# Performance work log

Measured on AMD Instinct MI355X. Metric: run time of the kernel, lower is better.

## Reference

```python
import jax, jax.numpy as jnp
import numpy as np

B, HP, WP, C = 64, 16, 32, 512   # batch, rows, cols, cnn_feature_size
H = 512                          # hidden_size
L = 2                            # num_layers
MAXH = 32


def setup_inputs() -> dict:
    key = jax.random.key(0)
    ks = jax.random.split(key, 11)
    s = 0.05  # keep gates out of saturation
    return {
        "features":   jax.random.normal(ks[0], (B, HP, WP, C), jnp.float32),
        "pos_emb_fw": jax.random.normal(ks[1], (MAXH + 1, L * 2 * H), jnp.float32) * s,
        "pos_emb_bw": jax.random.normal(ks[2], (MAXH + 1, L * 2 * H), jnp.float32) * s,
        "Wi_fw": jax.random.normal(ks[3], (L, C, 4 * H), jnp.float32) * s,
        "Wh_fw": jax.random.normal(ks[4], (L, H, 4 * H), jnp.float32) * s,
        "bi_fw": jax.random.normal(ks[5], (L, 4 * H), jnp.float32) * s,
        "bh_fw": jax.random.normal(ks[6], (L, 4 * H), jnp.float32) * s,
        "Wi_bw": jax.random.normal(ks[7], (L, C, 4 * H), jnp.float32) * s,
        "Wh_bw": jax.random.normal(ks[8], (L, H, 4 * H), jnp.float32) * s,
        "bi_bw": jax.random.normal(ks[9], (L, 4 * H), jnp.float32) * s,
        "bh_bw": jax.random.normal(ks[10], (L, 4 * H), jnp.float32) * s,
    }


def _stacked_lstm_scan(xs, h0, c0, Wi, Wh, b):
    """xs: (T, N, C); h0, c0: (L, N, H); returns (T, N, H) top-layer outputs."""
    def step(carry, x_t):
        hs, cs = carry
        inp = x_t
        new_h, new_c = [], []
        for l in range(Wi.shape[0]):
            gates = inp @ Wi[l] + hs[l] @ Wh[l] + b[l]          # (N, 4H)
            i_g, f_g, o_g, g_g = jnp.split(gates, 4, axis=-1)   # gate order as in torch chunk
            c_n = jax.nn.sigmoid(f_g) * cs[l] + jax.nn.sigmoid(i_g) * jnp.tanh(g_g)
            h_n = jax.nn.sigmoid(o_g) * jnp.tanh(c_n)
            new_h.append(h_n); new_c.append(c_n)
            inp = h_n
        return (jnp.stack(new_h), jnp.stack(new_c)), inp
    _, ys = jax.lax.scan(step, (h0, c0), xs)
    return ys


def _init_state(pos_emb, row_idx, n, l, h):
    # pos_emb[row_idx]: (N, L*2*H) laid out as [h_1, c_1, ..., h_L, c_L]
    e = pos_emb[row_idx].reshape(n, l, 2, h)
    return e[:, :, 0].transpose(1, 0, 2), e[:, :, 1].transpose(1, 0, 2)  # (L, N, H) each


def reference(features, pos_emb_fw, pos_emb_bw,
              Wi_fw, Wh_fw, bi_fw, bh_fw,
              Wi_bw, Wh_bw, bi_bw, bh_bw):
    b, hp, wp, c = features.shape
    l, _, h4 = Wi_fw.shape
    h = h4 // 4
    n = b * hp  # rows are independent -> fuse into one scan batch

    # (B, Hp, Wp, C) -> (Wp, B*Hp, C), time-major
    xs = features.transpose(2, 0, 1, 3).reshape(wp, n, c)
    # row index i+1 per flattened (b, row) element
    row_idx = jnp.tile(jnp.arange(1, hp + 1), b)  # (N,)

    h0f, c0f = _init_state(pos_emb_fw, row_idx, n, l, h)
    out_fw = _stacked_lstm_scan(xs, h0f, c0f, Wi_fw, Wh_fw, bi_fw + bh_fw)

    h0b, c0b = _init_state(pos_emb_bw, row_idx, n, l, h)
    out_bw = jnp.flip(
        _stacked_lstm_scan(jnp.flip(xs, 0), h0b, c0b, Wi_bw, Wh_bw, bi_bw + bh_bw), 0)

    ctx = jnp.concatenate([out_fw, out_bw], axis=-1)        # (Wp, N, 2H)
    ctx = ctx.reshape(wp, b, hp, 2 * h).transpose(1, 2, 0, 3)  # (B, Hp, Wp, 2H)
    return ctx.reshape(b, hp * wp, 2 * h)
```

## Files before the change

kernel.cpp:

```cpp
#include <hip/hip_runtime.h>
#include <hip/hip_bf16.h>
#include <stdint.h>

#define B_    64
#define HP_   16
#define WP_   32
#define CH_   512
#define HS_   512
#define NSEQ  1024
#define G4    2048
#define KTOT  1024

typedef __hip_bfloat16 bf16_t;
typedef __bf16 bf16x8 __attribute__((ext_vector_type(8)));
typedef float  f32x4  __attribute__((ext_vector_type(4)));

#define WT_OFF   0
#define XBF_OFF  16777216
#define HBUF_OFF 50331648
#define CBUF_OFF 58720256
#define PB_OFF   67108864
#define HB_ELEMS (2*2*1024*512)

__device__ __forceinline__ float sigf(float x) {
    return 1.0f / (1.0f + __expf(-x));
}
__device__ __forceinline__ float tanhfast(float x) {
    x = fminf(fmaxf(x, -15.0f), 15.0f);
    float e = __expf(-2.0f * x);
    return (1.0f - e) / (1.0f + e);
}

__device__ __forceinline__ void gload16(const bf16_t* g, bf16_t* l) {
    __builtin_amdgcn_global_load_lds(
        (const __attribute__((address_space(1))) void*)g,
        (__attribute__((address_space(3))) void*)l, 16, 0, 0);
}

__global__ void k_prep_w(const float* __restrict__ Wi_fw, const float* __restrict__ Wh_fw,
                         const float* __restrict__ Wi_bw, const float* __restrict__ Wh_bw,
                         bf16_t* __restrict__ Wt) {
    int bxi = blockIdx.x;
    int cb = bxi & 63;
    int kb = (bxi >> 6) & 31;
    int u  = bxi >> 11;
    int l  = u >> 1, dir = u & 1;
    const float* Wi = dir ? Wi_bw : Wi_fw;
    const float* Wh = dir ? Wh_bw : Wh_fw;
    int k0 = kb * 32;
    const float* src = (k0 < 512) ? (Wi + (size_t)l*512*2048 + (size_t)k0*2048)
                                  : (Wh + (size_t)l*512*2048 + (size_t)(k0-512)*2048);
    int jblk = cb >> 2, g = cb & 3;
    int sc0 = g*512 + jblk*32;
    int cp0 = cb * 32;
    __shared__ float ld[32][33];
    int tx = threadIdx.x & 31, ty = threadIdx.x >> 5;
#pragma unroll
    for (int i = 0; i < 4; ++i) {
        int kr = ty + i*8;
        ld[kr][tx] = src[(size_t)kr*2048 + sc0 + tx];
    }
    __syncthreads();
#pragma unroll
    for (int i = 0; i < 4; ++i) {
        int cl = ty + i*8;
        Wt[((size_t)u*G4 + cp0 + cl)*KTOT + k0 + tx] = __float2bfloat16(ld[tx][cl]);
    }
}

__global__ void k_prep_bias(const float* __restrict__ bi_fw, const float* __restrict__ bh_fw,
                            const float* __restrict__ bi_bw, const float* __restrict__ bh_bw,
                            float* __restrict__ pb) {
    int id = blockIdx.x * 256 + threadIdx.x;
    if (id >= 4*G4) return;
    int u = id >> 11, cp = id & 2047;
    int l = u >> 1, dir = u & 1;
    int jblk = cp >> 7, rr = cp & 127, g = rr >> 5, jin = rr & 31;
    int col = g*512 + jblk*32 + jin;
    const float* bi = dir ? bi_bw : bi_fw;
    const float* bh = dir ? bh_bw : bh_fw;
    pb[id] = bi[l*G4 + col] + bh[l*G4 + col];
}

__global__ void k_convert_x(const float* __restrict__ f, bf16_t* __restrict__ xbf) {
    int id = blockIdx.x * 256 + threadIdx.x;
    int c8 = id & 63;
    int t  = (id >> 6) & 31;
    int n  = id >> 11;
    const float* s = f + ((size_t)n*WP_ + t)*CH_ + c8*8;
    bf16_t* d = xbf + ((size_t)t*NSEQ + n)*CH_ + c8*8;
#pragma unroll
    for (int i = 0; i < 8; ++i) d[i] = __float2bfloat16(s[i]);
}

__global__ void k_init_state(const float* __restrict__ pe_fw, const float* __restrict__ pe_bw,
                             bf16_t* __restrict__ hbuf, float* __restrict__ cbuf) {
    int id = blockIdx.x * 256 + threadIdx.x;
    int j = id & 511;
    int n = (id >> 9) & 1023;
    int l = (id >> 19) & 1;
    int dir = id >> 20;
    const float* pe = dir ? pe_bw : pe_fw;
    int rowi = (n & 15) + 1;
    float h = pe[(size_t)rowi*2048 + l*1024 + j];
    float c = pe[(size_t)rowi*2048 + l*1024 + 512 + j];
    int pp = (l == 0) ? 1 : 0;
    hbuf[(size_t)pp*HB_ELEMS + (((size_t)dir*2 + l)*NSEQ + n)*HS_ + j] = __float2bfloat16(h);
    cbuf[(((size_t)dir*2 + l)*NSEQ + n)*HS_ + j] = c;
}

__global__ __launch_bounds__(256, 2) void k_phase(
    int p,
    const bf16_t* __restrict__ xbf,
    const bf16_t* __restrict__ Wt,
    const float*  __restrict__ pb,
    bf16_t* __restrict__ hbuf,
    float*  __restrict__ cbuf,
    float*  __restrict__ out) {

    int bx = blockIdx.x;
    int xcd   = bx & 7;
    int layer = (bx >> 8) & 1;
    int r5    = (bx >> 3) & 31;
    int dir   = r5 & 1;
    int cb    = xcd * 2 + ((r5 >> 1) & 1);
    int rb    = r5 >> 2;
    int u     = layer * 2 + dir;

    if (layer == 0 && p >= WP_) return;
    if (layer == 1 && p < 1)    return;

    int row0 = rb * 128;
    int c0 = cb * 128;

    const bf16_t* hread = hbuf + (size_t)((p + 1) & 1) * HB_ELEMS;
    bf16_t* hwrite      = hbuf + (size_t)(p & 1) * HB_ELEMS;

    const bf16_t* A1;
    const bf16_t* A2;
    int t_out = 0;
    if (layer == 0) {
        int t = dir ? (WP_ - 1 - p) : p;
        A1 = xbf + (size_t)t * NSEQ * CH_;
        A2 = hread + ((size_t)dir*2 + 0) * NSEQ * HS_;
    } else {
        A1 = hread + ((size_t)dir*2 + 0) * NSEQ * HS_;
        A2 = hread + ((size_t)dir*2 + 1) * NSEQ * HS_;
        t_out = dir ? (WP_ - p) : (p - 1);
    }
    const bf16_t* Wu = Wt + (size_t)u * G4 * KTOT;

    __shared__ __align__(16) bf16_t a_lds[2][128*64];
    __shared__ __align__(16) bf16_t b_lds[2][128*64];

    int tid = threadIdx.x;
    int lane = tid & 63;
    int wv = tid >> 6;

    f32x4 acc[2][8];
#pragma unroll
    for (int m = 0; m < 2; ++m)
#pragma unroll
        for (int n = 0; n < 8; ++n)
            acc[m][n] = (f32x4){0.f, 0.f, 0.f, 0.f};

    auto STAGE = [&](int kt, int bufi) {
        const bf16_t* Asrc;
        int kloc;
        if (kt < 8) { Asrc = A1; kloc = kt * 64; }
        else        { Asrc = A2; kloc = kt * 64 - 512; }
#pragma unroll
        for (int q = 0; q < 4; ++q) {
            int id = q*256 + tid;
            int r = id >> 3;
            int s = id & 7;
            int kk = ((s ^ (r & 7)) << 3);
            gload16(Asrc + (size_t)(row0 + r)*512 + kloc + kk,
                    a_lds[bufi] + (size_t)(q*256 + (wv << 6)) * 8);
        }
#pragma unroll
        for (int q = 0; q < 4; ++q) {
            int id = q*256 + tid;
            int r = id >> 3;
            int s = id & 7;
            int kk = ((s ^ (r & 7)) << 3);
            gload16(Wu + (size_t)(c0 + r)*KTOT + kt*64 + kk,
                    b_lds[bufi] + (size_t)(q*256 + (wv << 6)) * 8);
        }
    };

    auto COMPUTE = [&](int bufi) {
        const char* ac = (const char*)a_lds[bufi];
        const char* bc = (const char*)b_lds[bufi];
#pragma unroll
        for (int ks = 0; ks < 2; ++ks) {
            int kb = (ks << 5) + ((lane >> 4) << 3);
            bf16x8 av[2], bv[8];
#pragma unroll
            for (int m = 0; m < 2; ++m) {
                int row = (wv << 5) + (m << 4) + (lane & 15);
                int byte = row*128 + kb*2;
                byte ^= (row & 7) << 4;
                av[m] = *(const bf16x8*)(ac + byte);
            }
#pragma unroll
            for (int n = 0; n < 8; ++n) {
                int colr = (n << 4) + (lane & 15);
                int byte = colr*128 + kb*2;
                byte ^= (colr & 7) << 4;
                bv[n] = *(const bf16x8*)(bc + byte);
            }
#pragma unroll
            for (int m = 0; m < 2; ++m)
#pragma unroll
                for (int n = 0; n < 8; ++n)
                    acc[m][n] = __builtin_amdgcn_mfma_f32_16x16x32_bf16(av[m], bv[n], acc[m][n], 0, 0, 0);
        }
    };

    STAGE(0, 0);
    int cur = 0;
    for (int kt = 0; kt < 15; ++kt) {
        STAGE(kt + 1, cur ^ 1);
        asm volatile("s_waitcnt vmcnt(8)" ::: "memory");
        __builtin_amdgcn_s_barrier();
        COMPUTE(cur);
        __builtin_amdgcn_s_barrier();
        cur ^= 1;
    }
    asm volatile("s_waitcnt vmcnt(0)" ::: "memory");
    __builtin_amdgcn_s_barrier();
    COMPUTE(cur);

    float bias[4][2];
#pragma unroll
    for (int g = 0; g < 4; ++g)
#pragma unroll
        for (int jq = 0; jq < 2; ++jq)
            bias[g][jq] = pb[u*G4 + c0 + g*32 + jq*16 + (lane & 15)];

    float* cptr = cbuf + ((size_t)dir*2 + layer) * NSEQ * HS_;
    bf16_t* hw  = hwrite + ((size_t)dir*2 + layer) * NSEQ * HS_;

#pragma unroll
    for (int m = 0; m < 2; ++m) {
#pragma unroll
        for (int jq = 0; jq < 2; ++jq) {
            f32x4 iv = acc[m][0 + jq];
            f32x4 fv = acc[m][2 + jq];
            f32x4 ov = acc[m][4 + jq];
            f32x4 gv = acc[m][6 + jq];
            int j = cb*32 + jq*16 + (lane & 15);
#pragma unroll
            for (int r = 0; r < 4; ++r) {
                int row = (wv << 5) + (m << 4) + ((lane >> 4) << 2) + r;
                int n = row0 + row;
                float ig = sigf(iv[r] + bias[0][jq]);
                float fg = sigf(fv[r] + bias[1][jq]);
                float og = sigf(ov[r] + bias[2][jq]);
                float gg = tanhfast(gv[r] + bias[3][jq]);
                size_t sidx = (size_t)n * HS_ + j;
                float cp = cptr[sidx];
                float cn = fg * cp + ig * gg;
                float hn = og * tanhfast(cn);
                cptr[sidx] = cn;
                hw[sidx] = __float2bfloat16(hn);
                if (layer == 1)
                    out[((size_t)n * WP_ + t_out) * (2*HS_) + (size_t)dir*HS_ + j] = hn;
            }
        }
    }
}

extern "C" void kernel_launch(void* const* d_in, const int* in_sizes, int n_in,
                              void* d_out, int out_size, void* d_ws, size_t ws_size,
                              hipStream_t stream) {
    const float* features = (const float*)d_in[0];
    const float* pe_fw = (const float*)d_in[1];
    const float* pe_bw = (const float*)d_in[2];
    const float* Wi_fw = (const float*)d_in[3];
    const float* Wh_fw = (const float*)d_in[4];
    const float* bi_fw = (const float*)d_in[5];
    const float* bh_fw = (const float*)d_in[6];
    const float* Wi_bw = (const float*)d_in[7];
    const float* Wh_bw = (const float*)d_in[8];
    const float* bi_bw = (const float*)d_in[9];
    const float* bh_bw = (const float*)d_in[10];

    char* ws = (char*)d_ws;
    bf16_t* Wt   = (bf16_t*)(ws + WT_OFF);
    bf16_t* xbf  = (bf16_t*)(ws + XBF_OFF);
    bf16_t* hbuf = (bf16_t*)(ws + HBUF_OFF);
    float*  cbuf = (float*)(ws + CBUF_OFF);
    float*  pb   = (float*)(ws + PB_OFF);
    float*  out  = (float*)d_out;

    k_prep_w<<<dim3(8192), dim3(256), 0, stream>>>(Wi_fw, Wh_fw, Wi_bw, Wh_bw, Wt);
    k_prep_bias<<<dim3(32), dim3(256), 0, stream>>>(bi_fw, bh_fw, bi_bw, bh_bw, pb);
    k_convert_x<<<dim3(8192), dim3(256), 0, stream>>>(features, xbf);
    k_init_state<<<dim3(8192), dim3(256), 0, stream>>>(pe_fw, pe_bw, hbuf, cbuf);

    for (int p = 0; p <= WP_; ++p)
        k_phase<<<dim3(512), dim3(256), 0, stream>>>(p, xbf, Wt, pb, hbuf, cbuf, out);
}
```

Baseline: 1.134 ms.

## Replace per-step kernel launches with persistent kernel and grid-wide atomic barrier

```diff
diff --git a/kernel.cpp b/kernel.cpp
--- a/kernel.cpp
+++ b/kernel.cpp
@@ -20,6 +20,7 @@
 #define HBUF_OFF 50331648
 #define CBUF_OFF 58720256
 #define PB_OFF   67108864
+#define CNT_OFF  (PB_OFF + 32768)
 #define HB_ELEMS (2*2*1024*512)
 
 __device__ __forceinline__ float sigf(float x) {
@@ -70,8 +71,9 @@
 
 __global__ void k_prep_bias(const float* __restrict__ bi_fw, const float* __restrict__ bh_fw,
                             const float* __restrict__ bi_bw, const float* __restrict__ bh_bw,
-                            float* __restrict__ pb) {
+                            float* __restrict__ pb, uint32_t* __restrict__ cnt) {
     int id = blockIdx.x * 256 + threadIdx.x;
+    if (id == 0) *cnt = 0;
     if (id >= 4*G4) return;
     int u = id >> 11, cp = id & 2047;
     int l = u >> 1, dir = u & 1;
@@ -109,14 +111,14 @@
     cbuf[(((size_t)dir*2 + l)*NSEQ + n)*HS_ + j] = c;
 }
 
-__global__ __launch_bounds__(256, 2) void k_phase(
-    int p,
+__global__ __launch_bounds__(256, 2) void k_persist(
     const bf16_t* __restrict__ xbf,
     const bf16_t* __restrict__ Wt,
     const float*  __restrict__ pb,
     bf16_t* __restrict__ hbuf,
     float*  __restrict__ cbuf,
-    float*  __restrict__ out) {
+    float*  __restrict__ out,
+    uint32_t* __restrict__ cnt) {
 
     int bx = blockIdx.x;
     int xcd   = bx & 7;
@@ -127,27 +129,9 @@
     int rb    = r5 >> 2;
     int u     = layer * 2 + dir;
 
-    if (layer == 0 && p >= WP_) return;
-    if (layer == 1 && p < 1)    return;
-
     int row0 = rb * 128;
     int c0 = cb * 128;
 
-    const bf16_t* hread = hbuf + (size_t)((p + 1) & 1) * HB_ELEMS;
-    bf16_t* hwrite      = hbuf + (size_t)(p & 1) * HB_ELEMS;
-
-    const bf16_t* A1;
-    const bf16_t* A2;
-    int t_out = 0;
-    if (layer == 0) {
-        int t = dir ? (WP_ - 1 - p) : p;
-        A1 = xbf + (size_t)t * NSEQ * CH_;
-        A2 = hread + ((size_t)dir*2 + 0) * NSEQ * HS_;
-    } else {
-        A1 = hread + ((size_t)dir*2 + 0) * NSEQ * HS_;
-        A2 = hread + ((size_t)dir*2 + 1) * NSEQ * HS_;
-        t_out = dir ? (WP_ - p) : (p - 1);
-    }
     const bf16_t* Wu = Wt + (size_t)u * G4 * KTOT;
 
     __shared__ __align__(16) bf16_t a_lds[2][128*64];
@@ -157,118 +141,150 @@
     int lane = tid & 63;
     int wv = tid >> 6;
 
-    f32x4 acc[2][8];
-#pragma unroll
-    for (int m = 0; m < 2; ++m)
-#pragma unroll
-        for (int n = 0; n < 8; ++n)
-            acc[m][n] = (f32x4){0.f, 0.f, 0.f, 0.f};
-
-    auto STAGE = [&](int kt, int bufi) {
-        const bf16_t* Asrc;
-        int kloc;
-        if (kt < 8) { Asrc = A1; kloc = kt * 64; }
-        else        { Asrc = A2; kloc = kt * 64 - 512; }
-#pragma unroll
-        for (int q = 0; q < 4; ++q) {
-            int id = q*256 + tid;
-            int r = id >> 3;
-            int s = id & 7;
-            int kk = ((s ^ (r & 7)) << 3);
-            gload16(Asrc + (size_t)(row0 + r)*512 + kloc + kk,
-                    a_lds[bufi] + (size_t)(q*256 + (wv << 6)) * 8);
-        }
-#pragma unroll
-        for (int q = 0; q < 4; ++q) {
-            int id = q*256 + tid;
-            int r = id >> 3;
-            int s = id & 7;
-            int kk = ((s ^ (r & 7)) << 3);
-            gload16(Wu + (size_t)(c0 + r)*KTOT + kt*64 + kk,
-                    b_lds[bufi] + (size_t)(q*256 + (wv << 6)) * 8);
-        }
-    };
-
-    auto COMPUTE = [&](int bufi) {
-        const char* ac = (const char*)a_lds[bufi];
-        const char* bc = (const char*)b_lds[bufi];
-#pragma unroll
-        for (int ks = 0; ks < 2; ++ks) {
-            int kb = (ks << 5) + ((lane >> 4) << 3);
-            bf16x8 av[2], bv[8];
-#pragma unroll
-            for (int m = 0; m < 2; ++m) {
-                int row = (wv << 5) + (m << 4) + (lane & 15);
-                int byte = row*128 + kb*2;
-                byte ^= (row & 7) << 4;
-                av[m] = *(const bf16x8*)(ac + byte);
-            }
-#pragma unroll
-            for (int n = 0; n < 8; ++n) {
-                int colr = (n << 4) + (lane & 15);
-                int byte = colr*128 + kb*2;
-                byte ^= (colr & 7) << 4;
-                bv[n] = *(const bf16x8*)(bc + byte);
-            }
-#pragma unroll
-            for (int m = 0; m < 2; ++m)
-#pragma unroll
-                for (int n = 0; n < 8; ++n)
-                    acc[m][n] = __builtin_amdgcn_mfma_f32_16x16x32_bf16(av[m], bv[n], acc[m][n], 0, 0, 0);
-        }
-    };
-
-    STAGE(0, 0);
-    int cur = 0;
-    for (int kt = 0; kt < 15; ++kt) {
-        STAGE(kt + 1, cur ^ 1);
-        asm volatile("s_waitcnt vmcnt(8)" ::: "memory");
-        __builtin_amdgcn_s_barrier();
-        COMPUTE(cur);
-        __builtin_amdgcn_s_barrier();
-        cur ^= 1;
-    }
-    asm volatile("s_waitcnt vmcnt(0)" ::: "memory");
-    __builtin_amdgcn_s_barrier();
-    COMPUTE(cur);
-
     float bias[4][2];
 #pragma unroll
     for (int g = 0; g < 4; ++g)
 #pragma unroll
         for (int jq = 0; jq < 2; ++jq)
             bias[g][jq] = pb[u*G4 + c0 + g*32 + jq*16 + (lane & 15)];
-
     float* cptr = cbuf + ((size_t)dir*2 + layer) * NSEQ * HS_;
-    bf16_t* hw  = hwrite + ((size_t)dir*2 + layer) * NSEQ * HS_;
-
-#pragma unroll
-    for (int m = 0; m < 2; ++m) {
-#pragma unroll
-        for (int jq = 0; jq < 2; ++jq) {
-            f32x4 iv = acc[m][0 + jq];
-            f32x4 fv = acc[m][2 + jq];
-            f32x4 ov = acc[m][4 + jq];
-            f32x4 gv = acc[m][6 + jq];
-            int j = cb*32 + jq*16 + (lane & 15);
-#pragma unroll
-            for (int r = 0; r < 4; ++r) {
-                int row = (wv << 5) + (m << 4) + ((lane >> 4) << 2) + r;
-                int n = row0 + row;
-                float ig = sigf(iv[r] + bias[0][jq]);
-                float fg = sigf(fv[r] + bias[1][jq]);
-                float og = sigf(ov[r] + bias[2][jq]);
-                float gg = tanhfast(gv[r] + bias[3][jq]);
-                size_t sidx = (size_t)n * HS_ + j;
-                float cp = cptr[sidx];
-                float cn = fg * cp + ig * gg;
-                float hn = og * tanhfast(cn);
-                cptr[sidx] = cn;
-                hw[sidx] = __float2bfloat16(hn);
-                if (layer == 1)
-                    out[((size_t)n * WP_ + t_out) * (2*HS_) + (size_t)dir*HS_ + j] = hn;
+
+#pragma unroll 1
+    for (int p = 0; p <= WP_; ++p) {
+        bool active = !(layer == 0 && p >= WP_) && !(layer == 1 && p < 1);
+        if (active) {
+            const bf16_t* hread = hbuf + (size_t)((p + 1) & 1) * HB_ELEMS;
+            bf16_t* hwrite      = hbuf + (size_t)(p & 1) * HB_ELEMS;
+
+            const bf16_t* A1;
+            const bf16_t* A2;
+            int t_out = 0;
+            if (layer == 0) {
+                int t = dir ? (WP_ - 1 - p) : p;
+                A1 = xbf + (size_t)t * NSEQ * CH_;
+                A2 = hread + ((size_t)dir*2 + 0) * NSEQ * HS_;
+            } else {
+                A1 = hread + ((size_t)dir*2 + 0) * NSEQ * HS_;
+                A2 = hread + ((size_t)dir*2 + 1) * NSEQ * HS_;
+                t_out = dir ? (WP_ - p) : (p - 1);
+            }
+
+            f32x4 acc[2][8];
+#pragma unroll
+            for (int m = 0; m < 2; ++m)
+#pragma unroll
+                for (int n = 0; n < 8; ++n)
+                    acc[m][n] = (f32x4){0.f, 0.f, 0.f, 0.f};
+
+            auto STAGE = [&](int kt, int bufi) {
+                const bf16_t* Asrc;
+                int kloc;
+                if (kt < 8) { Asrc = A1; kloc = kt * 64; }
+                else        { Asrc = A2; kloc = kt * 64 - 512; }
+#pragma unroll
+                for (int q = 0; q < 4; ++q) {
+                    int id = q*256 + tid;
+                    int r = id >> 3;
+                    int s = id & 7;
+                    int kk = ((s ^ (r & 7)) << 3);
+                    gload16(Asrc + (size_t)(row0 + r)*512 + kloc + kk,
+                            a_lds[bufi] + (size_t)(q*256 + (wv << 6)) * 8);
+                }
+#pragma unroll
+                for (int q = 0; q < 4; ++q) {
+                    int id = q*256 + tid;
+                    int r = id >> 3;
+                    int s = id & 7;
+                    int kk = ((s ^ (r & 7)) << 3);
+                    gload16(Wu + (size_t)(c0 + r)*KTOT + kt*64 + kk,
+                            b_lds[bufi] + (size_t)(q*256 + (wv << 6)) * 8);
+                }
+            };
+
+            auto COMPUTE = [&](int bufi) {
+                const char* ac = (const char*)a_lds[bufi];
+                const char* bc = (const char*)b_lds[bufi];
+#pragma unroll
+                for (int ks = 0; ks < 2; ++ks) {
+                    int kb = (ks << 5) + ((lane >> 4) << 3);
+                    bf16x8 av[2], bv[8];
+#pragma unroll
+                    for (int m = 0; m < 2; ++m) {
+                        int row = (wv << 5) + (m << 4) + (lane & 15);
+                        int byte = row*128 + kb*2;
+                        byte ^= (row & 7) << 4;
+                        av[m] = *(const bf16x8*)(ac + byte);
+                    }
+#pragma unroll
+                    for (int n = 0; n < 8; ++n) {
+                        int colr = (n << 4) + (lane & 15);
+                        int byte = colr*128 + kb*2;
+                        byte ^= (colr & 7) << 4;
+                        bv[n] = *(const bf16x8*)(bc + byte);
+                    }
+#pragma unroll
+                    for (int m = 0; m < 2; ++m)
+#pragma unroll
+                        for (int n = 0; n < 8; ++n)
+                            acc[m][n] = __builtin_amdgcn_mfma_f32_16x16x32_bf16(av[m], bv[n], acc[m][n], 0, 0, 0);
+                }
+            };
+
+            STAGE(0, 0);
+            int cur = 0;
+#pragma unroll 1
+            for (int kt = 0; kt < 15; ++kt) {
+                STAGE(kt + 1, cur ^ 1);
+                asm volatile("s_waitcnt vmcnt(8)" ::: "memory");
+                __builtin_amdgcn_s_barrier();
+                COMPUTE(cur);
+                __builtin_amdgcn_s_barrier();
+                cur ^= 1;
+            }
+            asm volatile("s_waitcnt vmcnt(0)" ::: "memory");
+            __builtin_amdgcn_s_barrier();
+            COMPUTE(cur);
+
+            bf16_t* hw = hwrite + ((size_t)dir*2 + layer) * NSEQ * HS_;
+#pragma unroll
+            for (int m = 0; m < 2; ++m) {
+#pragma unroll
+                for (int jq = 0; jq < 2; ++jq) {
+                    f32x4 iv = acc[m][0 + jq];
+                    f32x4 fv = acc[m][2 + jq];
+                    f32x4 ov = acc[m][4 + jq];
+                    f32x4 gv = acc[m][6 + jq];
+                    int j = cb*32 + jq*16 + (lane & 15);
+#pragma unroll
+                    for (int r = 0; r < 4; ++r) {
+                        int row = (wv << 5) + (m << 4) + ((lane >> 4) << 2) + r;
+                        int n = row0 + row;
+                        float ig = sigf(iv[r] + bias[0][jq]);
+                        float fg = sigf(fv[r] + bias[1][jq]);
+                        float og = sigf(ov[r] + bias[2][jq]);
+                        float gg = tanhfast(gv[r] + bias[3][jq]);
+                        size_t sidx = (size_t)n * HS_ + j;
+                        float cp = cptr[sidx];
+                        float cn = fg * cp + ig * gg;
+                        float hn = og * tanhfast(cn);
+                        cptr[sidx] = cn;
+                        hw[sidx] = __float2bfloat16(hn);
+                        if (layer == 1)
+                            out[((size_t)n * WP_ + t_out) * (2*HS_) + (size_t)dir*HS_ + j] = hn;
+                    }
+                }
             }
         }
+
+        __syncthreads();
+        if (tid == 0) {
+            __threadfence();
+            __hip_atomic_fetch_add(cnt, 1u, __ATOMIC_RELEASE, __HIP_MEMORY_SCOPE_AGENT);
+            uint32_t target = (uint32_t)(p + 1) * 512u;
+            while (__hip_atomic_load(cnt, __ATOMIC_ACQUIRE, __HIP_MEMORY_SCOPE_AGENT) < target)
+                __builtin_amdgcn_s_sleep(2);
+        }
+        __syncthreads();
     }
 }
 
@@ -293,13 +309,13 @@
     bf16_t* hbuf = (bf16_t*)(ws + HBUF_OFF);
     float*  cbuf = (float*)(ws + CBUF_OFF);
     float*  pb   = (float*)(ws + PB_OFF);
+    uint32_t* cnt = (uint32_t*)(ws + CNT_OFF);
     float*  out  = (float*)d_out;
 
     k_prep_w<<<dim3(8192), dim3(256), 0, stream>>>(Wi_fw, Wh_fw, Wi_bw, Wh_bw, Wt);
-    k_prep_bias<<<dim3(32), dim3(256), 0, stream>>>(bi_fw, bh_fw, bi_bw, bh_bw, pb);
+    k_prep_bias<<<dim3(32), dim3(256), 0, stream>>>(bi_fw, bh_fw, bi_bw, bh_bw, pb, cnt);
     k_convert_x<<<dim3(8192), dim3(256), 0, stream>>>(features, xbf);
     k_init_state<<<dim3(8192), dim3(256), 0, stream>>>(pe_fw, pe_bw, hbuf, cbuf);
 
-    for (int p = 0; p <= WP_; ++p)
-        k_phase<<<dim3(512), dim3(256), 0, stream>>>(p, xbf, Wt, pb, hbuf, cbuf, out);
-}
+    k_persist<<<dim3(512), dim3(256), 0, stream>>>(xbf, Wt, pb, hbuf, cbuf, out, cnt);
+}
```

After: 3.304 ms. 2.91x slower.

## Split 128x128 tile across eight waves instead of four in LSTM phase kernel

Applied to the files above, without the earlier changes.

```diff
diff --git a/kernel.cpp b/kernel.cpp
--- a/kernel.cpp
+++ b/kernel.cpp
@@ -109,7 +109,7 @@
     cbuf[(((size_t)dir*2 + l)*NSEQ + n)*HS_ + j] = c;
 }
 
-__global__ __launch_bounds__(256, 2) void k_phase(
+__global__ __launch_bounds__(512, 4) void k_phase(
     int p,
     const bf16_t* __restrict__ xbf,
     const bf16_t* __restrict__ Wt,
@@ -157,12 +157,10 @@
     int lane = tid & 63;
     int wv = tid >> 6;
 
-    f32x4 acc[2][8];
-#pragma unroll
-    for (int m = 0; m < 2; ++m)
-#pragma unroll
-        for (int n = 0; n < 8; ++n)
-            acc[m][n] = (f32x4){0.f, 0.f, 0.f, 0.f};
+    f32x4 acc[8];
+#pragma unroll
+    for (int n = 0; n < 8; ++n)
+        acc[n] = (f32x4){0.f, 0.f, 0.f, 0.f};
 
     auto STAGE = [&](int kt, int bufi) {
         const bf16_t* Asrc;
@@ -170,22 +168,22 @@
         if (kt < 8) { Asrc = A1; kloc = kt * 64; }
         else        { Asrc = A2; kloc = kt * 64 - 512; }
 #pragma unroll
-        for (int q = 0; q < 4; ++q) {
-            int id = q*256 + tid;
+        for (int q = 0; q < 2; ++q) {
+            int id = q*512 + tid;
             int r = id >> 3;
             int s = id & 7;
             int kk = ((s ^ (r & 7)) << 3);
             gload16(Asrc + (size_t)(row0 + r)*512 + kloc + kk,
-                    a_lds[bufi] + (size_t)(q*256 + (wv << 6)) * 8);
-        }
-#pragma unroll
-        for (int q = 0; q < 4; ++q) {
-            int id = q*256 + tid;
+                    a_lds[bufi] + (size_t)(q*512 + (wv << 6)) * 8);
+        }
+#pragma unroll
+        for (int q = 0; q < 2; ++q) {
+            int id = q*512 + tid;
             int r = id >> 3;
             int s = id & 7;
             int kk = ((s ^ (r & 7)) << 3);
             gload16(Wu + (size_t)(c0 + r)*KTOT + kt*64 + kk,
-                    b_lds[bufi] + (size_t)(q*256 + (wv << 6)) * 8);
+                    b_lds[bufi] + (size_t)(q*512 + (wv << 6)) * 8);
         }
     };
 
@@ -195,13 +193,12 @@
 #pragma unroll
         for (int ks = 0; ks < 2; ++ks) {
             int kb = (ks << 5) + ((lane >> 4) << 3);
-            bf16x8 av[2], bv[8];
-#pragma unroll
-            for (int m = 0; m < 2; ++m) {
-                int row = (wv << 5) + (m << 4) + (lane & 15);
+            bf16x8 av, bv[8];
+            {
+                int row = (wv << 4) + (lane & 15);
                 int byte = row*128 + kb*2;
                 byte ^= (row & 7) << 4;
-                av[m] = *(const bf16x8*)(ac + byte);
+                av = *(const bf16x8*)(ac + byte);
             }
 #pragma unroll
             for (int n = 0; n < 8; ++n) {
@@ -211,10 +208,8 @@
                 bv[n] = *(const bf16x8*)(bc + byte);
             }
 #pragma unroll
-            for (int m = 0; m < 2; ++m)
-#pragma unroll
-                for (int n = 0; n < 8; ++n)
-                    acc[m][n] = __builtin_amdgcn_mfma_f32_16x16x32_bf16(av[m], bv[n], acc[m][n], 0, 0, 0);
+            for (int n = 0; n < 8; ++n)
+                acc[n] = __builtin_amdgcn_mfma_f32_16x16x32_bf16(av, bv[n], acc[n], 0, 0, 0);
         }
     };
 
@@ -222,7 +217,7 @@
     int cur = 0;
     for (int kt = 0; kt < 15; ++kt) {
         STAGE(kt + 1, cur ^ 1);
-        asm volatile("s_waitcnt vmcnt(8)" ::: "memory");
+        asm volatile("s_waitcnt vmcnt(4)" ::: "memory");
         __builtin_amdgcn_s_barrier();
         COMPUTE(cur);
         __builtin_amdgcn_s_barrier();
@@ -243,31 +238,28 @@
     bf16_t* hw  = hwrite + ((size_t)dir*2 + layer) * NSEQ * HS_;
 
 #pragma unroll
-    for (int m = 0; m < 2; ++m) {
-#pragma unroll
-        for (int jq = 0; jq < 2; ++jq) {
-            f32x4 iv = acc[m][0 + jq];
-            f32x4 fv = acc[m][2 + jq];
-            f32x4 ov = acc[m][4 + jq];
-            f32x4 gv = acc[m][6 + jq];
-            int j = cb*32 + jq*16 + (lane & 15);
-#pragma unroll
-            for (int r = 0; r < 4; ++r) {
-                int row = (wv << 5) + (m << 4) + ((lane >> 4) << 2) + r;
-                int n = row0 + row;
-                float ig = sigf(iv[r] + bias[0][jq]);
-                float fg = sigf(fv[r] + bias[1][jq]);
-                float og = sigf(ov[r] + bias[2][jq]);
-                float gg = tanhfast(gv[r] + bias[3][jq]);
-                size_t sidx = (size_t)n * HS_ + j;
-                float cp = cptr[sidx];
-                float cn = fg * cp + ig * gg;
-                float hn = og * tanhfast(cn);
-                cptr[sidx] = cn;
-                hw[sidx] = __float2bfloat16(hn);
-                if (layer == 1)
-                    out[((size_t)n * WP_ + t_out) * (2*HS_) + (size_t)dir*HS_ + j] = hn;
-            }
+    for (int jq = 0; jq < 2; ++jq) {
+        f32x4 iv = acc[0 + jq];
+        f32x4 fv = acc[2 + jq];
+        f32x4 ov = acc[4 + jq];
+        f32x4 gv = acc[6 + jq];
+        int j = cb*32 + jq*16 + (lane & 15);
+#pragma unroll
+        for (int r = 0; r < 4; ++r) {
+            int row = (wv << 4) + ((lane >> 4) << 2) + r;
+            int n = row0 + row;
+            float ig = sigf(iv[r] + bias[0][jq]);
+            float fg = sigf(fv[r] + bias[1][jq]);
+            float og = sigf(ov[r] + bias[2][jq]);
+            float gg = tanhfast(gv[r] + bias[3][jq]);
+            size_t sidx = (size_t)n * HS_ + j;
+            float cp = cptr[sidx];
+            float cn = fg * cp + ig * gg;
+            float hn = og * tanhfast(cn);
+            cptr[sidx] = cn;
+            hw[sidx] = __float2bfloat16(hn);
+            if (layer == 1)
+                out[((size_t)n * WP_ + t_out) * (2*HS_) + (size_t)dir*HS_ + j] = hn;
         }
     }
 }
@@ -301,5 +293,5 @@
     k_init_state<<<dim3(8192), dim3(256), 0, stream>>>(pe_fw, pe_bw, hbuf, cbuf);
 
     for (int p = 0; p <= WP_; ++p)
-        k_phase<<<dim3(512), dim3(256), 0, stream>>>(p, xbf, Wt, pb, hbuf, cbuf, out);
-}
+        k_phase<<<dim3(512), dim3(512), 0, stream>>>(p, xbf, Wt, pb, hbuf, cbuf, out);
+}
```

After: 1.079 ms. -4.9%, faster.
